# Performance work log

Measured on AMD Instinct MI355X. Metric: run time of the kernel, lower is better.

## Reference

```python
import jax, jax.numpy as jnp
import numpy as np

TEMP = 10.0  # softmax temperature (self.Temp)
N_CENTERS = 16

def setup_inputs() -> dict:
    key = jax.random.key(0)
    k1, k2 = jax.random.split(key)
    x = jax.random.normal(k1, (16, 64, 128, 128), dtype=jnp.float32)
    center = jax.random.normal(k2, (N_CENTERS,), dtype=jnp.float32)
    return {"x": x, "center": center}

def reference(x, center):
    # Soft quantization branch (Q_type='Soft') with straight-through estimator.
    # diff[..., m] = x - center[m]  (broadcast instead of torch.stack)
    diff = x[..., None] - center  # [*, K]
    W_index = jnp.argmin(jnp.abs(diff), axis=-1)  # [*]
    W_hard = center[W_index]  # [*]
    smx = jax.nn.softmax(-TEMP * diff * diff, axis=-1)  # [*, K]
    W_soft = jnp.einsum('ijklm,m->ijkl', smx, center)  # [*]
    w_bias = jax.lax.stop_gradient(W_hard - W_soft)
    return w_bias + W_soft
```

## Files before the change

kernel.cpp:

```cpp
#include <hip/hip_runtime.h>
#include <hip/hip_bf16.h>
#include <math.h>

#define N_CENTERS 16
#define B_LUT 256

typedef float nfloat4 __attribute__((ext_vector_type(4)));


__device__ __forceinline__ void quant4(const float4 v,
                                       const float2* __restrict__ slut,
                                       float invw, float nb,
                                       nfloat4& rr, bool& bad)
{
    float xs[4] = {v.x, v.y, v.z, v.w};
    float r[4];
#pragma unroll
    for (int j = 0; j < 4; ++j) {
        float ft = fmaf(xs[j], invw, nb);
        ft = __builtin_amdgcn_fmed3f(ft, 0.f, (float)(B_LUT - 1));
        int t = (int)ft;
        float2 e = slut[t];
        float da = fabsf(xs[j] - e.x);
        float db = fabsf(xs[j] - e.y);
        r[j] = (db < da) ? e.y : e.x;
        bad |= (e.x != e.x);
    }
    rr = (nfloat4){r[0], r[1], r[2], r[3]};
}

__device__ __forceinline__ float4 exact4(const float4 v,
                                         const float* __restrict__ center)
{
    float xs[4] = {v.x, v.y, v.z, v.w};
    float r[4];
#pragma unroll
    for (int j = 0; j < 4; ++j) {
        float xv = xs[j];
        float best = fabsf(xv - center[0]);
        float bc = center[0];
#pragma unroll
        for (int m = 1; m < N_CENTERS; ++m) {
            float d = fabsf(xv - center[m]);
            bool lt = d < best;
            best = lt ? d : best;
            bc = lt ? center[m] : bc;
        }
        r[j] = bc;
    }
    return make_float4(r[0], r[1], r[2], r[3]);
}

__global__ void __launch_bounds__(256) quantizer_kernel(
    const float* __restrict__ x,
    const float* __restrict__ center,
    float* __restrict__ out,
    int q)
{
    __shared__ __align__(16) float2 slut[B_LUT];

    const float4* __restrict__ x4 = reinterpret_cast<const float4*>(x);
    float4* __restrict__ o4 = reinterpret_cast<float4*>(out);
    nfloat4* __restrict__ o4n = reinterpret_cast<nfloat4*>(out);

    int i = blockIdx.x * blockDim.x + threadIdx.x;

    float4 v0 = x4[i];
    float4 v1 = x4[i + q];
    float4 v2 = x4[i + 2 * q];
    float4 v3 = x4[i + 3 * q];

    float s[N_CENTERS];
#pragma unroll
    for (int m = 0; m < N_CENTERS; ++m) s[m] = center[m];
#pragma unroll
    for (int a = 0; a < N_CENTERS - 1; ++a)
#pragma unroll
        for (int j = 0; j < N_CENTERS - 1 - a; ++j) {
            float u = fminf(s[j], s[j + 1]);
            float vmx = fmaxf(s[j], s[j + 1]);
            s[j] = u; s[j + 1] = vmx;
        }

    float lo = s[0], hi = s[N_CENTERS - 1];
    float span = hi - lo;
    if (!(span > 0.f)) span = 1.f;
    float w = span / (float)B_LUT;
    float invw = (float)B_LUT / span;
    float nb = -lo * invw;

    {
        int t = threadIdx.x;
        float bstart = lo + t * w;
        float bend = bstart + w;
        float g = 0.02f * w;

        float mid[N_CENTERS - 1];
#pragma unroll
        for (int j = 0; j < N_CENTERS - 1; ++j) mid[j] = 0.5f * (s[j] + s[j + 1]);

        int cnt = 0, j0 = 0;
#pragma unroll
        for (int j = 0; j < N_CENTERS - 1; ++j) {
            bool inb = (mid[j] >= bstart - g) && (mid[j] < bend + g);
            if (inb) { if (cnt == 0) j0 = j; cnt++; }
        }

        float ca, cb;
        if (cnt == 0) {
            int k = 0;
#pragma unroll
            for (int j = 0; j < N_CENTERS - 1; ++j) k += (mid[j] < bstart) ? 1 : 0;
            float ck = s[0];
#pragma unroll
            for (int j = 1; j < N_CENTERS; ++j) ck = (j == k) ? s[j] : ck;
            ca = ck; cb = ck;
        } else if (cnt == 1) {
            float a = s[0], b = s[1];
#pragma unroll
            for (int j = 0; j < N_CENTERS - 1; ++j)
                if (j == j0) { a = s[j]; b = s[j + 1]; }
            int ia = N_CENTERS - 1, ib = N_CENTERS - 1;
#pragma unroll
            for (int m = N_CENTERS - 1; m >= 0; --m) {
                float cm = center[m];
                if (cm == a) ia = m;
                if (cm == b) ib = m;
            }
            if (ia <= ib) { ca = a; cb = b; } else { ca = b; cb = a; }
        } else {
            ca = __uint_as_float(0x7fc00000u);
            cb = 0.f;
        }
        slut[t] = make_float2(ca, cb);
    }
    __syncthreads();

    bool bad = false;
    nfloat4 r0, r1, r2, r3;
    quant4(v0, slut, invw, nb, r0, bad);
    quant4(v1, slut, invw, nb, r1, bad);
    quant4(v2, slut, invw, nb, r2, bad);
    quant4(v3, slut, invw, nb, r3, bad);

    __builtin_nontemporal_store(r0, &o4n[i]);
    __builtin_nontemporal_store(r1, &o4n[i + q]);
    __builtin_nontemporal_store(r2, &o4n[i + 2 * q]);
    __builtin_nontemporal_store(r3, &o4n[i + 3 * q]);

    if (__any(bad)) {
        float4 e0 = exact4(x4[i], center);
        float4 e1 = exact4(x4[i + q], center);
        float4 e2 = exact4(x4[i + 2 * q], center);
        float4 e3 = exact4(x4[i + 3 * q], center);
        o4[i]         = e0;
        o4[i + q]     = e1;
        o4[i + 2 * q] = e2;
        o4[i + 3 * q] = e3;
    }
}

extern "C" void kernel_launch(void* const* d_in, const int* in_sizes, int n_in,
                              void* d_out, int out_size, void* d_ws, size_t ws_size,
                              hipStream_t stream) {
    const float* x      = (const float*)d_in[0];
    const float* center = (const float*)d_in[1];
    float* out          = (float*)d_out;

    int n = in_sizes[0];
    int n4 = n / 4;
    int q  = n4 / 4;

    const int block = 256;
    int grid = q / block;
    quantizer_kernel<<<grid, block, 0, stream>>>(x, center, out, q);
}
```

Measured before the change: 27.90 us.

## Process eight float4 per thread and build sorted centers via shared rank sort

Each thread now handles eight float4 vectors instead of four, which halves the grid and amortizes the per-block lookup-table construction over more elements. The per-thread register bubble sort of the 16 centers is replaced by a rank sort done by 16 threads into shared memory, which stores original indices for tie ordering and adds one extra barrier. LUT bin classification now uses prefix counts instead of per-midpoint scans. The cost is more registers for the eight in-flight loads and fewer blocks to hide latency.

```diff
diff --git a/kernel.cpp b/kernel.cpp
--- a/kernel.cpp
+++ b/kernel.cpp
@@ -2,32 +2,11 @@
 #include <hip/hip_bf16.h>
 #include <math.h>
 
-#define N_CENTERS 16
+#define NC 16
 #define B_LUT 256
 
 typedef float nfloat4 __attribute__((ext_vector_type(4)));
 
-
-__device__ __forceinline__ void quant4(const float4 v,
-                                       const float2* __restrict__ slut,
-                                       float invw, float nb,
-                                       nfloat4& rr, bool& bad)
-{
-    float xs[4] = {v.x, v.y, v.z, v.w};
-    float r[4];
-#pragma unroll
-    for (int j = 0; j < 4; ++j) {
-        float ft = fmaf(xs[j], invw, nb);
-        ft = __builtin_amdgcn_fmed3f(ft, 0.f, (float)(B_LUT - 1));
-        int t = (int)ft;
-        float2 e = slut[t];
-        float da = fabsf(xs[j] - e.x);
-        float db = fabsf(xs[j] - e.y);
-        r[j] = (db < da) ? e.y : e.x;
-        bad |= (e.x != e.x);
-    }
-    rr = (nfloat4){r[0], r[1], r[2], r[3]};
-}
 
 __device__ __forceinline__ float4 exact4(const float4 v,
                                          const float* __restrict__ center)
@@ -40,7 +19,7 @@
         float best = fabsf(xv - center[0]);
         float bc = center[0];
 #pragma unroll
-        for (int m = 1; m < N_CENTERS; ++m) {
+        for (int m = 1; m < NC; ++m) {
             float d = fabsf(xv - center[m]);
             bool lt = d < best;
             best = lt ? d : best;
@@ -58,6 +37,8 @@
     int q)
 {
     __shared__ __align__(16) float2 slut[B_LUT];
+    __shared__ float ssort[NC];
+    __shared__ int   sidx[NC];
 
     const float4* __restrict__ x4 = reinterpret_cast<const float4*>(x);
     float4* __restrict__ o4 = reinterpret_cast<float4*>(out);
@@ -65,69 +46,60 @@
 
     int i = blockIdx.x * blockDim.x + threadIdx.x;
 
-    float4 v0 = x4[i];
-    float4 v1 = x4[i + q];
-    float4 v2 = x4[i + 2 * q];
-    float4 v3 = x4[i + 3 * q];
+    float4 v[8];
+#pragma unroll
+    for (int k = 0; k < 8; ++k) v[k] = x4[i + k * q];
 
-    float s[N_CENTERS];
+    if (threadIdx.x < NC) {
+        int t = (int)threadIdx.x;
+        float c = center[t];
+        int rank = 0;
 #pragma unroll
-    for (int m = 0; m < N_CENTERS; ++m) s[m] = center[m];
-#pragma unroll
-    for (int a = 0; a < N_CENTERS - 1; ++a)
-#pragma unroll
-        for (int j = 0; j < N_CENTERS - 1 - a; ++j) {
-            float u = fminf(s[j], s[j + 1]);
-            float vmx = fmaxf(s[j], s[j + 1]);
-            s[j] = u; s[j + 1] = vmx;
+        for (int m = 0; m < NC; ++m) {
+            float cm = center[m];
+            rank += (cm < c || (cm == c && m < t)) ? 1 : 0;
         }
+        ssort[rank] = c;
+        sidx[rank] = t;
+    }
+    __syncthreads();
 
-    float lo = s[0], hi = s[N_CENTERS - 1];
-    float span = hi - lo;
+    float s0 = ssort[0], s15 = ssort[NC - 1];
+    float span = s15 - s0;
     if (!(span > 0.f)) span = 1.f;
-    float w = span / (float)B_LUT;
-    float invw = (float)B_LUT / span;
-    float nb = -lo * invw;
+    float w = span * (1.0f / 256.0f);
+    float invw = 256.0f / span;
+    float nb = -s0 * invw;
 
     {
-        int t = threadIdx.x;
-        float bstart = lo + t * w;
-        float bend = bstart + w;
+        int t = (int)threadIdx.x;
+        float bstart = s0 + t * w;
         float g = 0.02f * w;
+        float lo_th = bstart - g;
+        float hi_th = bstart + w + g;
 
-        float mid[N_CENTERS - 1];
+        int k0 = 0, k1 = 0;
+        float sp = s0;
 #pragma unroll
-        for (int j = 0; j < N_CENTERS - 1; ++j) mid[j] = 0.5f * (s[j] + s[j + 1]);
-
-        int cnt = 0, j0 = 0;
-#pragma unroll
-        for (int j = 0; j < N_CENTERS - 1; ++j) {
-            bool inb = (mid[j] >= bstart - g) && (mid[j] < bend + g);
-            if (inb) { if (cnt == 0) j0 = j; cnt++; }
+        for (int j = 0; j < NC - 1; ++j) {
+            float sn = ssort[j + 1];
+            float mid = 0.5f * (sp + sn);
+            k0 += (mid < lo_th) ? 1 : 0;
+            k1 += (mid < hi_th) ? 1 : 0;
+            sp = sn;
         }
+        int cnt = k1 - k0;
 
         float ca, cb;
         if (cnt == 0) {
-            int k = 0;
-#pragma unroll
-            for (int j = 0; j < N_CENTERS - 1; ++j) k += (mid[j] < bstart) ? 1 : 0;
-            float ck = s[0];
-#pragma unroll
-            for (int j = 1; j < N_CENTERS; ++j) ck = (j == k) ? s[j] : ck;
+            float ck = ssort[k0];
             ca = ck; cb = ck;
         } else if (cnt == 1) {
-            float a = s[0], b = s[1];
-#pragma unroll
-            for (int j = 0; j < N_CENTERS - 1; ++j)
-                if (j == j0) { a = s[j]; b = s[j + 1]; }
-            int ia = N_CENTERS - 1, ib = N_CENTERS - 1;
-#pragma unroll
-            for (int m = N_CENTERS - 1; m >= 0; --m) {
-                float cm = center[m];
-                if (cm == a) ia = m;
-                if (cm == b) ib = m;
-            }
-            if (ia <= ib) { ca = a; cb = b; } else { ca = b; cb = a; }
+            float a = ssort[k0], b = ssort[k0 + 1];
+            int ia = sidx[k0], ib = sidx[k0 + 1];
+            bool sw = ib < ia;
+            ca = sw ? b : a;
+            cb = sw ? a : b;
         } else {
             ca = __uint_as_float(0x7fc00000u);
             cb = 0.f;
@@ -137,26 +109,29 @@
     __syncthreads();
 
     bool bad = false;
-    nfloat4 r0, r1, r2, r3;
-    quant4(v0, slut, invw, nb, r0, bad);
-    quant4(v1, slut, invw, nb, r1, bad);
-    quant4(v2, slut, invw, nb, r2, bad);
-    quant4(v3, slut, invw, nb, r3, bad);
-
-    __builtin_nontemporal_store(r0, &o4n[i]);
-    __builtin_nontemporal_store(r1, &o4n[i + q]);
-    __builtin_nontemporal_store(r2, &o4n[i + 2 * q]);
-    __builtin_nontemporal_store(r3, &o4n[i + 3 * q]);
+#pragma unroll
+    for (int k = 0; k < 8; ++k) {
+        float xs[4] = {v[k].x, v[k].y, v[k].z, v[k].w};
+        float r[4];
+#pragma unroll
+        for (int j = 0; j < 4; ++j) {
+            float ft = fmaf(xs[j], invw, nb);
+            ft = __builtin_amdgcn_fmed3f(ft, 0.f, (float)(B_LUT - 1));
+            int t = (int)ft;
+            float2 e = slut[t];
+            float da = fabsf(xs[j] - e.x);
+            float db = fabsf(xs[j] - e.y);
+            r[j] = (db < da) ? e.y : e.x;
+            bad |= (e.x != e.x);
+        }
+        __builtin_nontemporal_store((nfloat4){r[0], r[1], r[2], r[3]},
+                                    &o4n[i + k * q]);
+    }
 
     if (__any(bad)) {
-        float4 e0 = exact4(x4[i], center);
-        float4 e1 = exact4(x4[i + q], center);
-        float4 e2 = exact4(x4[i + 2 * q], center);
-        float4 e3 = exact4(x4[i + 3 * q], center);
-        o4[i]         = e0;
-        o4[i + q]     = e1;
-        o4[i + 2 * q] = e2;
-        o4[i + 3 * q] = e3;
+#pragma unroll
+        for (int k = 0; k < 8; ++k)
+            o4[i + k * q] = exact4(x4[i + k * q], center);
     }
 }
 
@@ -169,7 +144,7 @@
 
     int n = in_sizes[0];
     int n4 = n / 4;
-    int q  = n4 / 4;
+    int q  = n4 / 8;
 
     const int block = 256;
     int grid = q / block;
```

Result: no change. 28.00 us (+0.4%).
